# Kernel optimization log

Hardware: AMD Instinct MI355X
Metric: run time of the kernel (lower is better)

The kernel has to match this reference:

```python
import jax, jax.numpy as jnp
import numpy as np

# ---- hyperparameters (from init_kwargs) ----
B, SEQ, D_MODEL = 2, 2048, 1024
D_STATE, D_CONV, EXPAND, HEAD_DIM, CHUNK = 128, 4, 2, 64, 256
D_INNER = EXPAND * D_MODEL            # 2048
NH = D_INNER // HEAD_DIM              # 32 heads
CONV_DIM = D_INNER + 2 * D_STATE      # 2304
D_IN_PROJ = 2 * D_INNER + 2 * D_STATE + NH  # z, xBC, dt -> 4384
D_FF = 4 * D_MODEL
EPS = 1e-12


def setup_inputs() -> dict:
    key = jax.random.key(0)
    ks = jax.random.split(key, 16)
    s = 0.02
    f32 = jnp.float32
    inp = {
        "x": jax.random.normal(ks[0], (B, SEQ, D_MODEL), f32),
        "time_diff": jax.random.uniform(ks[1], (B, SEQ), f32),
        # TiSSD (Mamba2-style) params
        "W_in": jax.random.normal(ks[2], (D_MODEL, D_IN_PROJ), f32) * s,
        "b_in": jnp.zeros((D_IN_PROJ,), f32),
        "conv_w": jax.random.normal(ks[3], (CONV_DIM, D_CONV), f32) * s,
        "conv_b": jnp.zeros((CONV_DIM,), f32),
        "A_log": jnp.log(jnp.arange(1, NH + 1, dtype=f32)),
        "dt_bias": jnp.full((NH,), -2.0, f32),
        "D": jnp.ones((NH,), f32),
        "time_decay": jnp.full((NH,), -3.0, f32),   # time-aware decay rates
        "rms_w": jnp.ones((D_INNER,), f32),
        "W_out": jax.random.normal(ks[4], (D_INNER, D_MODEL), f32) * s,
        "b_out": jnp.zeros((D_MODEL,), f32),
        # wrapper LayerNorm
        "ln_g": jnp.ones((D_MODEL,), f32),
        "ln_b": jnp.zeros((D_MODEL,), f32),
        # FFN
        "fc1_w": jax.random.normal(ks[5], (D_MODEL, D_FF), f32) * s,
        "fc1_b": jnp.zeros((D_FF,), f32),
        "fc2_w": jax.random.normal(ks[6], (D_FF, D_MODEL), f32) * s,
        "fc2_b": jnp.zeros((D_MODEL,), f32),
        "ln2_g": jnp.ones((D_MODEL,), f32),
        "ln2_b": jnp.zeros((D_MODEL,), f32),
    }
    return inp


def _layer_norm(x, g, b, eps=EPS):
    mu = jnp.mean(x, axis=-1, keepdims=True)
    var = jnp.mean(jnp.square(x - mu), axis=-1, keepdims=True)
    return (x - mu) * jax.lax.rsqrt(var + eps) * g + b


def _hardswish(x):
    return x * jnp.clip(x + 3.0, 0.0, 6.0) * (1.0 / 6.0)


def _tissd_forward(x, time_diff, W_in, b_in, conv_w, conv_b, A_log, dt_bias, D,
                   time_decay, rms_w, W_out, b_out):
    b, l, _ = x.shape
    zxbcdt = x @ W_in + b_in                       # [b,l,D_IN_PROJ]
    z = zxbcdt[..., :D_INNER]
    xBC = zxbcdt[..., D_INNER:D_INNER + CONV_DIM]
    dt_raw = zxbcdt[..., -NH:]

    # causal depthwise conv1d (small fixed kernel -> unrolled shifts)
    xp = jnp.pad(xBC, ((0, 0), (D_CONV - 1, 0), (0, 0)))
    xBC_c = conv_b
    for k in range(D_CONV):
        xBC_c = xBC_c + xp[:, k:k + l, :] * conv_w[:, k]
    xBC_c = jax.nn.silu(xBC_c)

    xs = xBC_c[..., :D_INNER]
    Bm = xBC_c[..., D_INNER:D_INNER + D_STATE]     # [b,l,n]
    Cm = xBC_c[..., -D_STATE:]                     # [b,l,n]

    dt = jax.nn.softplus(dt_raw + dt_bias)         # [b,l,h]
    A = -jnp.exp(A_log)                            # [h]
    # time-aware: extra decay proportional to time gap
    dA = dt * A - jax.nn.softplus(time_decay) * time_diff[..., None]  # [b,l,h]

    xh = xs.reshape(b, l, NH, HEAD_DIM)
    xdt = xh * dt[..., None]                       # [b,l,h,p]

    nc = l // CHUNK
    xc = xdt.reshape(b, nc, CHUNK, NH, HEAD_DIM)
    Bc = Bm.reshape(b, nc, CHUNK, D_STATE)
    Cc = Cm.reshape(b, nc, CHUNK, D_STATE)
    dAc = dA.reshape(b, nc, CHUNK, NH).transpose(0, 3, 1, 2)  # [b,h,c,L]

    A_cum = jnp.cumsum(dAc, axis=-1)               # [b,h,c,L]
    seg = A_cum[..., :, None] - A_cum[..., None, :]
    mask = jnp.tril(jnp.ones((CHUNK, CHUNK), bool))
    Lmat = jnp.where(mask, jnp.exp(jnp.where(mask, seg, 0.0)), 0.0)  # [b,h,c,L,L]

    # intra-chunk (diagonal block) output
    Y_diag = jnp.einsum("bcln,bcsn,bhcls,bcshp->bclhp", Cc, Bc, Lmat, xc)

    # per-chunk final states
    decay_states = jnp.exp(A_cum[..., -1:] - A_cum)  # [b,h,c,L]
    states = jnp.einsum("bcln,bhcl,bclhp->bchpn", Bc, decay_states, xc)
    chunk_decay = jnp.exp(A_cum[..., -1])            # [b,h,c]

    # inter-chunk recurrence over nc chunks
    states_t = states.transpose(1, 0, 2, 3, 4)       # [c,b,h,p,n]
    decay_t = chunk_decay.transpose(2, 0, 1)         # [c,b,h]

    def step(carry, inp):
        s_c, d_c = inp
        new = carry * d_c[..., None, None] + s_c
        return new, carry                            # emit state BEFORE chunk

    init = jnp.zeros((b, NH, HEAD_DIM, D_STATE), x.dtype)
    _, prev_states = jax.lax.scan(step, init, (states_t, decay_t))
    prev_states = prev_states.transpose(1, 0, 2, 3, 4)  # [b,c,h,p,n]

    state_decay = jnp.exp(A_cum)                     # [b,h,c,L]
    Y_off = jnp.einsum("bcln,bchpn,bhcl->bclhp", Cc, prev_states, state_decay)

    Y = (Y_diag + Y_off).reshape(b, l, NH, HEAD_DIM) + D[None, None, :, None] * xh
    y = Y.reshape(b, l, D_INNER)

    # gated RMSNorm
    y = y * jax.nn.silu(z)
    y = y * jax.lax.rsqrt(jnp.mean(jnp.square(y), axis=-1, keepdims=True) + EPS) * rms_w
    return y @ W_out + b_out


def reference(x, time_diff, W_in, b_in, conv_w, conv_b, A_log, dt_bias, D,
              time_decay, rms_w, W_out, b_out, ln_g, ln_b,
              fc1_w, fc1_b, fc2_w, fc2_b, ln2_g, ln2_b):
    hidden = _tissd_forward(x, time_diff, W_in, b_in, conv_w, conv_b, A_log,
                            dt_bias, D, time_decay, rms_w, W_out, b_out)
    # num_layers > 1 -> residual; dropout is identity in eval mode
    h = _layer_norm(hidden + x, ln_g, ln_b)
    # FFN with Hardswish and residual LayerNorm
    hid = _hardswish(h @ fc1_w + fc1_b)
    hid = hid @ fc2_w + fc2_b
    out = _layer_norm(hid + h, ln2_g, ln2_b)
    return (out, time_diff)
```

## Files before the change

kernel.cpp:

```cpp
#include <hip/hip_runtime.h>

#define BATCH 2
#define SEQL 2048
#define DM 1024
#define DSTATE 128
#define HD 64
#define CHUNK 256
#define DI 2048
#define NHEADS 32
#define CONVD 2304
#define DPROJ 4384
#define DFF 4096
#define NC 8
#define ROWS (BATCH*SEQL)

typedef unsigned short ushort_t;
typedef short bf16x8 __attribute__((ext_vector_type(8)));
typedef float f32x4 __attribute__((ext_vector_type(4)));

__device__ __forceinline__ float softplus_f(float v){
    return (v > 20.f) ? v : log1pf(expf(v));
}
__device__ __forceinline__ float silu_f(float v){
    return v / (1.f + expf(-v));
}
__device__ __forceinline__ ushort_t f2b(float v){
    union { float f; unsigned int u; } x; x.f = v;
    unsigned int r = x.u + 0x7fffu + ((x.u >> 16) & 1u);
    return (ushort_t)(r >> 16);
}
__device__ __forceinline__ float b2f(ushort_t v){
    union { unsigned int u; float f; } x; x.u = ((unsigned int)v) << 16;
    return x.f;
}

template<int ACT, int OUT_BF16, int TN, int NS, int DTX>
__global__ __launch_bounds__(256) void mfma_gemm_k(
    const ushort_t* __restrict__ A, const ushort_t* __restrict__ Bt,
    const float* __restrict__ bias, float* __restrict__ Cf,
    ushort_t* __restrict__ Cb, float* __restrict__ dtaux,
    int M, int N, int K, int ldc)
{
    constexpr int NT = (TN == 128) ? 4 : 2;
    constexpr int BROWS = TN / 4;
    __shared__ ushort_t As[128*64];
    __shared__ ushort_t Bs[TN*64];
    int tid = threadIdx.x;
    int lane = tid & 63, wave = tid >> 6;
    int m0 = blockIdx.y * 128, n0 = blockIdx.x * TN;
    int Ks = K / NS;
    int kb = (NS > 1) ? blockIdx.z * Ks : 0;
    int wave_m = (TN==128) ? (wave >> 1)*64 : (wave & 1)*64;
    int wave_n = (TN==128) ? (wave & 1)*64 : (wave >> 1)*32;
    int lrow = lane >> 3;
    int lcol = ((lane & 7) ^ lrow) * 8;
    const ushort_t* Abase = A  + (size_t)(m0 + wave*32    + lrow)*K + lcol + kb;
    const ushort_t* Bbase = Bt + (size_t)(n0 + wave*BROWS + lrow)*K + lcol + kb;
    ushort_t* AsW = &As[(wave*32)*64];
    ushort_t* BsW = &Bs[(wave*BROWS)*64];
    f32x4 acc[4][NT];
    #pragma unroll
    for (int i=0;i<4;i++)
        #pragma unroll
        for (int j=0;j<NT;j++) acc[i][j] = (f32x4){0.f,0.f,0.f,0.f};
    int lm = lane & 15;
    int quad = lane >> 4;
    for (int k0 = 0; k0 < Ks; k0 += 64){
        #pragma unroll
        for (int j = 0; j < 4; j++)
            __builtin_amdgcn_global_load_lds(
                (const __attribute__((address_space(1))) void*)(Abase + (size_t)(j*8)*K + k0),
                (__attribute__((address_space(3))) void*)(AsW + j*8*64), 16, 0, 0);
        #pragma unroll
        for (int j = 0; j < BROWS/8; j++)
            __builtin_amdgcn_global_load_lds(
                (const __attribute__((address_space(1))) void*)(Bbase + (size_t)(j*8)*K + k0),
                (__attribute__((address_space(3))) void*)(BsW + j*8*64), 16, 0, 0);
        __syncthreads();
        #pragma unroll
        for (int kk = 0; kk < 64; kk += 32){
            int cb = kk >> 3;
            bf16x8 af[4], bfr[NT];
            #pragma unroll
            for (int mt=0; mt<4; mt++)
                af[mt] = *(const bf16x8*)&As[(wave_m + mt*16 + lm)*64 + (((cb + quad) ^ (lm & 7))*8)];
            #pragma unroll
            for (int nt=0; nt<NT; nt++)
                bfr[nt] = *(const bf16x8*)&Bs[(wave_n + nt*16 + lm)*64 + (((cb + quad) ^ (lm & 7))*8)];
            #pragma unroll
            for (int mt=0; mt<4; mt++)
                #pragma unroll
                for (int nt=0; nt<NT; nt++)
                    acc[mt][nt] = __builtin_amdgcn_mfma_f32_16x16x32_bf16(af[mt], bfr[nt], acc[mt][nt], 0, 0, 0);
        }
        __syncthreads();
    }
    float* Cfo = Cf + (size_t)((NS > 1) ? blockIdx.z : 0) * (size_t)M * ldc;
    int addb = (NS == 1) || (blockIdx.z == 0);
    int crow0 = m0 + wave_m + quad * 4;
    int ccol0 = n0 + wave_n + lm;
    #pragma unroll
    for (int mt=0; mt<4; mt++){
        #pragma unroll
        for (int nt=0; nt<NT; nt++){
            int col = ccol0 + nt*16;
            if (col < N){
                float bv = addb ? bias[col] : 0.f;
                #pragma unroll
                for (int r=0; r<4; r++){
                    int row = crow0 + mt*16 + r;
                    float v = acc[mt][nt][r] + bv;
                    if (ACT == 1){
                        float t = fminf(fmaxf(v + 3.f, 0.f), 6.f);
                        v = v * t * (1.f/6.f);
                    }
                    if (OUT_BF16){
                        Cb[(size_t)row*ldc + col] = f2b(v);
                        if (DTX && col >= N - NHEADS)
                            dtaux[(size_t)row*NHEADS + (col - (N - NHEADS))] = v;
                    } else {
                        Cfo[(size_t)row*ldc + col] = v;
                    }
                }
            }
        }
    }
}

__global__ __launch_bounds__(256) void prep_in_k(const float* __restrict__ x,
                                                 ushort_t* __restrict__ x_bf,
                                                 const float* __restrict__ W_in,
                                                 ushort_t* __restrict__ WinT){
    __shared__ ushort_t tile[32][33];
    int bid = blockIdx.x;
    if (bid < 16384){
        int idx = bid*256 + threadIdx.x;
        x_bf[idx] = f2b(x[idx]);
        return;
    }
    int id2 = bid - 16384;
    int n0 = (id2 % 140)*32, k0 = (id2 / 140)*32;
    int tx = threadIdx.x & 31, ty = threadIdx.x >> 5;
    #pragma unroll
    for (int i = 0; i < 4; i++){
        int k = k0 + ty + i*8;
        int n = n0 + tx;
        float v = (n < DPROJ) ? W_in[(size_t)k*DPROJ + n] : 0.f;
        tile[ty + i*8][tx] = f2b(v);
    }
    __syncthreads();
    #pragma unroll
    for (int i = 0; i < 4; i++)
        WinT[(size_t)(n0 + ty + i*8)*DM + k0 + tx] = tile[tx][ty + i*8];
}

__global__ __launch_bounds__(256) void transpose3_k(const float* __restrict__ Wout,
                                                    const float* __restrict__ fc1w,
                                                    const float* __restrict__ fc2w,
                                                    ushort_t* __restrict__ WoutT,
                                                    ushort_t* __restrict__ fc1T,
                                                    ushort_t* __restrict__ fc2T){
    __shared__ ushort_t tile[32][33];
    int bid = blockIdx.x;
    const float* W; ushort_t* Wt; int K, N, gx, id;
    if (bid < 2048){        W = Wout; Wt = WoutT; K = DI;  N = DM;  gx = 32;  id = bid; }
    else if (bid < 6144){   W = fc1w; Wt = fc1T;  K = DM;  N = DFF; gx = 128; id = bid - 2048; }
    else {                  W = fc2w; Wt = fc2T;  K = DFF; N = DM;  gx = 32;  id = bid - 6144; }
    int n0 = (id % gx)*32, k0 = (id / gx)*32;
    int tx = threadIdx.x & 31, ty = threadIdx.x >> 5;
    #pragma unroll
    for (int i = 0; i < 4; i++){
        int k = k0 + ty + i*8;
        int n = n0 + tx;
        tile[ty + i*8][tx] = f2b(W[(size_t)k*N + n]);
    }
    __syncthreads();
    #pragma unroll
    for (int i = 0; i < 4; i++)
        Wt[(size_t)(n0 + ty + i*8)*K + k0 + tx] = tile[tx][ty + i*8];
}

#define CONVBLKS (ROWS*CONVD/256)
__global__ __launch_bounds__(256) void conv_dt_k(const ushort_t* __restrict__ zx,
                                                 const float* __restrict__ conv_w,
                                                 const float* __restrict__ conv_b,
                                                 ushort_t* __restrict__ convb,
                                                 const float* __restrict__ dtaux,
                                                 const float* __restrict__ time_diff,
                                                 const float* __restrict__ A_log,
                                                 const float* __restrict__ dt_bias,
                                                 const float* __restrict__ time_decay,
                                                 float* __restrict__ dtH,
                                                 float* __restrict__ Acum){
    __shared__ float s[CHUNK];
    int bid = blockIdx.x;
    if (bid < CONVBLKS){
        int idx = bid*256 + threadIdx.x;
        int c = idx % CONVD;
        int row = idx / CONVD;
        int t = row & (SEQL-1);
        float acc = conv_b[c];
        #pragma unroll
        for (int k = 0; k < 4; k++){
            int tt = t + k - 3;
            if (tt >= 0)
                acc += b2f(zx[((size_t)(row + k - 3))*DPROJ + DI + c]) * conv_w[c*4 + k];
        }
        convb[idx] = f2b(silu_f(acc));
        return;
    }
    int id2 = bid - CONVBLKS;
    int c = id2 % NC;
    int h = (id2 / NC) % NHEADS;
    int b = id2 / (NC*NHEADS);
    int l = threadIdx.x;
    int t = c*CHUNK + l;
    float dtr = dtaux[((size_t)(b*SEQL + t))*NHEADS + h];
    float dtv = softplus_f(dtr + dt_bias[h]);
    float A = -expf(A_log[h]);
    float dA = dtv*A - softplus_f(time_decay[h]) * time_diff[b*SEQL + t];
    dtH[((size_t)(b*NHEADS + h))*SEQL + t] = dtv;
    s[l] = dA;
    __syncthreads();
    for (int off = 1; off < CHUNK; off <<= 1){
        float v = (l >= off) ? s[l-off] : 0.f;
        __syncthreads();
        s[l] += v;
        __syncthreads();
    }
    Acum[((size_t)(b*NHEADS + h))*SEQL + t] = s[l];
}

__global__ __launch_bounds__(256) void g_mfma_k(const ushort_t* __restrict__ convb,
                                                ushort_t* __restrict__ G){
    __shared__ ushort_t As[64*136];
    __shared__ ushort_t Bs[64*136];
    int bc = blockIdx.z;
    int l0 = blockIdx.y*64, s0 = blockIdx.x*64;
    int tid = threadIdx.x;
    int lane = tid & 63, wave = tid >> 6;
    int lm = lane & 15, quad = lane >> 4;
    const ushort_t* base = convb + (size_t)bc*CHUNK*CONVD;
    #pragma unroll
    for (int i = 0; i < 4; i++){
        int e = tid + i*256;
        int r = e >> 4, k = (e & 15)*8;
        *(bf16x8*)&As[r*136 + k] = *(const bf16x8*)&base[(size_t)(l0+r)*CONVD + DI + DSTATE + k];
        *(bf16x8*)&Bs[r*136 + k] = *(const bf16x8*)&base[(size_t)(s0+r)*CONVD + DI + k];
    }
    __syncthreads();
    f32x4 acc[4];
    #pragma unroll
    for (int j=0;j<4;j++) acc[j] = (f32x4){0.f,0.f,0.f,0.f};
    #pragma unroll
    for (int kk = 0; kk < 4; kk++){
        bf16x8 af = *(const bf16x8*)&As[(wave*16+lm)*136 + kk*32 + quad*8];
        #pragma unroll
        for (int nt = 0; nt < 4; nt++){
            bf16x8 bfr = *(const bf16x8*)&Bs[(nt*16+lm)*136 + kk*32 + quad*8];
            acc[nt] = __builtin_amdgcn_mfma_f32_16x16x32_bf16(af, bfr, acc[nt], 0, 0, 0);
        }
    }
    ushort_t* g = G + (size_t)bc*CHUNK*CHUNK;
    #pragma unroll
    for (int nt = 0; nt < 4; nt++)
        #pragma unroll
        for (int r = 0; r < 4; r++)
            g[(size_t)(l0 + wave*16 + quad*4 + r)*CHUNK + s0 + nt*16 + lm] = f2b(acc[nt][r]);
}

#define RSX 264
#define RSB 72
__global__ __launch_bounds__(256) void states_mfma_k(const ushort_t* __restrict__ convb,
                                                     const float* __restrict__ dtH,
                                                     const float* __restrict__ Acum,
                                                     float* __restrict__ states){
    __shared__ ushort_t xw[64*RSX];
    __shared__ ushort_t Bt[128*RSB];
    __shared__ float Acs[CHUNK];
    __shared__ float dts[CHUNK];
    int bid = blockIdx.x;
    int h = bid % NHEADS;
    int c = (bid / NHEADS) % NC;
    int b = bid / (NHEADS*NC);
    int tid = threadIdx.x;
    int lane = tid & 63, wave = tid >> 6;
    int lm = lane & 15, quad = lane >> 4;
    Acs[tid] = Acum[((size_t)(b*NHEADS + h))*SEQL + c*CHUNK + tid];
    dts[tid] = dtH[((size_t)(b*NHEADS + h))*SEQL + c*CHUNK + tid];
    __syncthreads();
    float AcL = Acs[CHUNK-1];
    {
        const ushort_t* xg = convb + ((size_t)(b*SEQL + c*CHUNK))*CONVD + h*HD;
        #pragma unroll
        for (int j8 = 0; j8 < 8; j8++){
            int s0 = wave*64 + j8*8;
            bf16x8 pk;
            #pragma unroll
            for (int j = 0; j < 8; j++){
                int l = s0 + j;
                pk[j] = (short)f2b(expf(AcL - Acs[l]) * dts[l] * b2f(xg[(size_t)l*CONVD + lane]));
            }
            *(bf16x8*)&xw[lane*RSX + s0] = pk;
        }
    }
    f32x4 acc[8];
    #pragma unroll
    for (int j=0;j<8;j++) acc[j] = (f32x4){0.f,0.f,0.f,0.f};
    const ushort_t* bbase = convb + ((size_t)(b*SEQL + c*CHUNK))*CONVD + DI;
    for (int l0 = 0; l0 < CHUNK; l0 += 64){
        __syncthreads();
        #pragma unroll
        for (int i = 0; i < 32; i++){
            int e = tid + i*256; int l = e >> 7, n = e & 127;
            Bt[n*RSB + l] = bbase[(size_t)(l0+l)*CONVD + n];
        }
        __syncthreads();
        #pragma unroll
        for (int kk = 0; kk < 2; kk++){
            bf16x8 af = *(const bf16x8*)&xw[(wave*16+lm)*RSX + l0 + kk*32 + quad*8];
            #pragma unroll
            for (int nt = 0; nt < 8; nt++){
                bf16x8 bfr = *(const bf16x8*)&Bt[(nt*16+lm)*RSB + kk*32 + quad*8];
                acc[nt] = __builtin_amdgcn_mfma_f32_16x16x32_bf16(af, bfr, acc[nt], 0, 0, 0);
            }
        }
    }
    float* outp = states + ((size_t)((b*NC + c)*NHEADS + h))*(HD*DSTATE);
    #pragma unroll
    for (int nt = 0; nt < 8; nt++)
        #pragma unroll
        for (int r = 0; r < 4; r++)
            outp[(size_t)(wave*16 + quad*4 + r)*DSTATE + nt*16 + lm] = acc[nt][r];
}

__global__ __launch_bounds__(256) void prev_scan_k(const float* __restrict__ states,
                                                   const float* __restrict__ Acum,
                                                   float* __restrict__ prev){
    int bid = blockIdx.x;
    int part = bid & 15;
    int h = (bid >> 4) & (NHEADS-1);
    int b = bid >> 9;
    int tid = threadIdx.x;
    const float* AcB = Acum + ((size_t)(b*NHEADS + h))*SEQL;
    float dec[NC];
    #pragma unroll
    for (int c = 0; c < NC; c++) dec[c] = expf(AcB[c*CHUNK + CHUNK-1]);
    #pragma unroll
    for (int j = 0; j < 2; j++){
        int e = part*512 + j*256 + tid;
        float carry = 0.f;
        #pragma unroll
        for (int c = 0; c < NC; c++){
            size_t idx = ((size_t)((b*NC + c)*NHEADS + h))*(HD*DSTATE) + e;
            prev[idx] = carry;
            carry = carry*dec[c] + states[idx];
        }
    }
}

#define RLX 264
#define RLP 136
__global__ __launch_bounds__(256) void y_mfma_k(const ushort_t* __restrict__ convb,
                                                const ushort_t* __restrict__ G,
                                                const float* __restrict__ Acum,
                                                const float* __restrict__ dtH,
                                                const float* __restrict__ prev,
                                                const float* __restrict__ Dp,
                                                ushort_t* __restrict__ Ybf){
    __shared__ ushort_t xdtT[64*RLX];
    __shared__ ushort_t prevs[64*RLP];
    __shared__ float Acs[CHUNK];
    __shared__ float dts[CHUNK];
    int bid = blockIdx.x;
    int h = bid % NHEADS;
    int c = (bid / NHEADS) % NC;
    int b = bid / (NHEADS*NC);
    int tid = threadIdx.x;
    int lane = tid & 63, wave = tid >> 6;
    int lm = lane & 15, quad = lane >> 4;

    Acs[tid] = Acum[((size_t)(b*NHEADS + h))*SEQL + c*CHUNK + tid];
    dts[tid] = dtH[((size_t)(b*NHEADS + h))*SEQL + c*CHUNK + tid];
    {
        const float* pv = prev + ((size_t)((b*NC + c)*NHEADS + h))*(HD*DSTATE);
        #pragma unroll
        for (int i = 0; i < 32; i++){
            int e = tid + i*256; int p = e >> 7, n = e & 127;
            prevs[p*RLP + n] = f2b(pv[e]);
        }
    }
    __syncthreads();
    {
        const ushort_t* xg = convb + ((size_t)(b*SEQL + c*CHUNK))*CONVD + h*HD;
        #pragma unroll
        for (int j8 = 0; j8 < 8; j8++){
            int s0 = wave*64 + j8*8;
            bf16x8 pk;
            #pragma unroll
            for (int j = 0; j < 8; j++){
                int l = s0 + j;
                pk[j] = (short)f2b(b2f(xg[(size_t)l*CONVD + lane]) * dts[l]);
            }
            *(bf16x8*)&xdtT[lane*RLX + s0] = pk;
        }
    }
    __syncthreads();

    int   lrow[4];  float Alr[4], eAlr[4];
    #pragma unroll
    for (int mt = 0; mt < 4; mt++){
        lrow[mt] = (mt*4 + wave)*16 + lm;
        Alr[mt]  = Acs[lrow[mt]];
        eAlr[mt] = expf(Alr[mt]);
    }
    const ushort_t* Gbase = G + ((size_t)(b*NC + c))*(CHUNK*CHUNK);

    f32x4 acc[4][4];
    #pragma unroll
    for (int i=0;i<4;i++)
        #pragma unroll
        for (int j=0;j<4;j++) acc[i][j] = (f32x4){0.f,0.f,0.f,0.f};

    for (int ks = 0; ks < 8; ks++){
        bf16x8 bfr[4];
        #pragma unroll
        for (int nt = 0; nt < 4; nt++)
            bfr[nt] = *(const bf16x8*)&xdtT[(nt*16+lm)*RLX + ks*32 + quad*8];
        #pragma unroll
        for (int mt = 0; mt < 4; mt++){
            int rblk = mt*4 + wave;
            int nst = rblk/2 + 1;
            if (ks < nst){
                int sbase = ks*32 + quad*8;
                bf16x8 g8 = *(const bf16x8*)&Gbase[(size_t)lrow[mt]*CHUNK + sbase];
                const float4* A4 = (const float4*)(&Acs[sbase]);
                float4 a0 = A4[0], a1 = A4[1];
                float Al = Alr[mt]; int l = lrow[mt];
                float pv[8];
                pv[0] = (sbase+0 <= l) ? b2f((ushort_t)g8[0])*expf(Al - a0.x) : 0.f;
                pv[1] = (sbase+1 <= l) ? b2f((ushort_t)g8[1])*expf(Al - a0.y) : 0.f;
                pv[2] = (sbase+2 <= l) ? b2f((ushort_t)g8[2])*expf(Al - a0.z) : 0.f;
                pv[3] = (sbase+3 <= l) ? b2f((ushort_t)g8[3])*expf(Al - a0.w) : 0.f;
                pv[4] = (sbase+4 <= l) ? b2f((ushort_t)g8[4])*expf(Al - a1.x) : 0.f;
                pv[5] = (sbase+5 <= l) ? b2f((ushort_t)g8[5])*expf(Al - a1.y) : 0.f;
                pv[6] = (sbase+6 <= l) ? b2f((ushort_t)g8[6])*expf(Al - a1.z) : 0.f;
                pv[7] = (sbase+7 <= l) ? b2f((ushort_t)g8[7])*expf(Al - a1.w) : 0.f;
                bf16x8 af;
                #pragma unroll
                for (int j = 0; j < 8; j++) af[j] = (short)f2b(pv[j]);
                #pragma unroll
                for (int nt = 0; nt < 4; nt++)
                    acc[mt][nt] = __builtin_amdgcn_mfma_f32_16x16x32_bf16(af, bfr[nt], acc[mt][nt], 0, 0, 0);
            }
        }
    }
    for (int kc = 0; kc < 4; kc++){
        bf16x8 bfr[4];
        #pragma unroll
        for (int nt = 0; nt < 4; nt++)
            bfr[nt] = *(const bf16x8*)&prevs[(nt*16+lm)*RLP + kc*32 + quad*8];
        #pragma unroll
        for (int mt = 0; mt < 4; mt++){
            int rowg = b*SEQL + c*CHUNK + lrow[mt];
            bf16x8 c8 = *(const bf16x8*)&convb[(size_t)rowg*CONVD + DI + DSTATE + kc*32 + quad*8];
            float e = eAlr[mt];
            bf16x8 af;
            #pragma unroll
            for (int j = 0; j < 8; j++) af[j] = (short)f2b(e * b2f((ushort_t)c8[j]));
            #pragma unroll
            for (int nt = 0; nt < 4; nt++)
                acc[mt][nt] = __builtin_amdgcn_mfma_f32_16x16x32_bf16(af, bfr[nt], acc[mt][nt], 0, 0, 0);
        }
    }
    float Dv = Dp[h];
    #pragma unroll
    for (int mt = 0; mt < 4; mt++){
        int l0 = (mt*4 + wave)*16 + quad*4;
        #pragma unroll
        for (int nt = 0; nt < 4; nt++){
            int p = nt*16 + lm;
            #pragma unroll
            for (int r = 0; r < 4; r++){
                int rowg = b*SEQL + c*CHUNK + l0 + r;
                float xs = b2f(convb[(size_t)rowg*CONVD + h*HD + p]);
                Ybf[(size_t)rowg*DI + h*HD + p] = f2b(acc[mt][nt][r] + Dv*xs);
            }
        }
    }
}

__global__ __launch_bounds__(256) void gate_rms_k(const ushort_t* __restrict__ Yb,
                                                  const ushort_t* __restrict__ zx,
                                                  const float* __restrict__ rms_w,
                                                  ushort_t* __restrict__ yn){
    __shared__ float red[4];
    __shared__ float scale_s;
    int row = blockIdx.x; int tid = threadIdx.x;
    float v[8]; float ss = 0.f;
    #pragma unroll
    for (int i = 0; i < 8; i++){
        int d = tid + i*256;
        float g = b2f(Yb[(size_t)row*DI + d]) * silu_f(b2f(zx[(size_t)row*DPROJ + d]));
        v[i] = g; ss += g*g;
    }
    #pragma unroll
    for (int off = 32; off > 0; off >>= 1) ss += __shfl_down(ss, off);
    int lane = tid & 63, wid = tid >> 6;
    if (lane == 0) red[wid] = ss;
    __syncthreads();
    if (tid == 0) scale_s = rsqrtf((red[0]+red[1]+red[2]+red[3])*(1.f/DI) + 1e-12f);
    __syncthreads();
    float sc = scale_s;
    #pragma unroll
    for (int i = 0; i < 8; i++){
        int d = tid + i*256;
        yn[(size_t)row*DI + d] = f2b(v[i]*sc*rms_w[d]);
    }
}

__global__ __launch_bounds__(256) void ln_hbf_k(const float* __restrict__ a,
                                                const float* __restrict__ a2,
                                                const float* __restrict__ resid,
                                                const float* __restrict__ g,
                                                const float* __restrict__ bw,
                                                ushort_t* __restrict__ bfout){
    __shared__ float redA[4], redB[4];
    __shared__ float mu_s, rs_s;
    int row = blockIdx.x; int tid = threadIdx.x;
    float u[4]; float s = 0.f, s2 = 0.f;
    #pragma unroll
    for (int i = 0; i < 4; i++){
        int d = tid + i*256;
        float val = a[(size_t)row*DM + d] + a2[(size_t)row*DM + d] + resid[(size_t)row*DM + d];
        u[i] = val; s += val; s2 += val*val;
    }
    #pragma unroll
    for (int off = 32; off > 0; off >>= 1){
        s  += __shfl_down(s,  off);
        s2 += __shfl_down(s2, off);
    }
    int lane = tid & 63, wid = tid >> 6;
    if (lane == 0){ redA[wid] = s; redB[wid] = s2; }
    __syncthreads();
    if (tid == 0){
        float S  = redA[0]+redA[1]+redA[2]+redA[3];
        float S2 = redB[0]+redB[1]+redB[2]+redB[3];
        float mu = S*(1.f/DM);
        float var = S2*(1.f/DM) - mu*mu;
        mu_s = mu; rs_s = rsqrtf(var + 1e-12f);
    }
    __syncthreads();
    float mu = mu_s, rs = rs_s;
    #pragma unroll
    for (int i = 0; i < 4; i++){
        int d = tid + i*256;
        bfout[(size_t)row*DM + d] = f2b((u[i]-mu)*rs*g[d] + bw[d]);
    }
}

__global__ __launch_bounds__(256) void ln_final_k(const float* __restrict__ a,
                                                  const float* __restrict__ a2,
                                                  const ushort_t* __restrict__ residb,
                                                  const float* __restrict__ g,
                                                  const float* __restrict__ bw,
                                                  float* __restrict__ outp,
                                                  const float* __restrict__ td){
    __shared__ float redA[4], redB[4];
    __shared__ float mu_s, rs_s;
    int row = blockIdx.x; int tid = threadIdx.x;
    if (row >= ROWS){
        int idx = (row - ROWS)*256 + tid;
        outp[(size_t)ROWS*DM + idx] = td[idx];
        return;
    }
    float u[4]; float s = 0.f, s2 = 0.f;
    #pragma unroll
    for (int i = 0; i < 4; i++){
        int d = tid + i*256;
        float val = a[(size_t)row*DM + d] + a2[(size_t)row*DM + d] + b2f(residb[(size_t)row*DM + d]);
        u[i] = val; s += val; s2 += val*val;
    }
    #pragma unroll
    for (int off = 32; off > 0; off >>= 1){
        s  += __shfl_down(s,  off);
        s2 += __shfl_down(s2, off);
    }
    int lane = tid & 63, wid = tid >> 6;
    if (lane == 0){ redA[wid] = s; redB[wid] = s2; }
    __syncthreads();
    if (tid == 0){
        float S  = redA[0]+redA[1]+redA[2]+redA[3];
        float S2 = redB[0]+redB[1]+redB[2]+redB[3];
        float mu = S*(1.f/DM);
        float var = S2*(1.f/DM) - mu*mu;
        mu_s = mu; rs_s = rsqrtf(var + 1e-12f);
    }
    __syncthreads();
    float mu = mu_s, rs = rs_s;
    #pragma unroll
    for (int i = 0; i < 4; i++){
        int d = tid + i*256;
        outp[(size_t)row*DM + d] = (u[i]-mu)*rs*g[d] + bw[d];
    }
}

extern "C" void kernel_launch(void* const* d_in, const int* in_sizes, int n_in,
                              void* d_out, int out_size, void* d_ws, size_t ws_size,
                              hipStream_t stream){
    const float* x         = (const float*)d_in[0];
    const float* time_diff = (const float*)d_in[1];
    const float* W_in      = (const float*)d_in[2];
    const float* b_in      = (const float*)d_in[3];
    const float* conv_w    = (const float*)d_in[4];
    const float* conv_b    = (const float*)d_in[5];
    const float* A_log     = (const float*)d_in[6];
    const float* dt_bias   = (const float*)d_in[7];
    const float* Dp        = (const float*)d_in[8];
    const float* time_dec  = (const float*)d_in[9];
    const float* rms_w     = (const float*)d_in[10];
    const float* W_out     = (const float*)d_in[11];
    const float* b_out     = (const float*)d_in[12];
    const float* ln_g      = (const float*)d_in[13];
    const float* ln_b      = (const float*)d_in[14];
    const float* fc1_w     = (const float*)d_in[15];
    const float* fc1_b     = (const float*)d_in[16];
    const float* fc2_w     = (const float*)d_in[17];
    const float* fc2_b     = (const float*)d_in[18];
    const float* ln2_g     = (const float*)d_in[19];
    const float* ln2_b     = (const float*)d_in[20];

    float* ws = (float*)d_ws;
    float* zx    = ws;
    float* convb = zx    + 17956864;
    float* dtH   = convb + 9437184;
    float* Acum  = dtH   + 131072;
    float* r4    = Acum  + 131072;
    float* r5    = r4    + 8388608;
    float* ybreg = r5    + 9437184;
    ushort_t* zx_bf  = (ushort_t*)zx;
    float*    dtaux  = zx + 10600000;
    ushort_t* mid_bf = (ushort_t*)zx;
    ushort_t* h_bf   = (ushort_t*)(zx + 8388608);
    ushort_t* convb_bf = (ushort_t*)convb;
    float* outPa  = convb;
    ushort_t* x_bf  = (ushort_t*)r4;
    ushort_t* WinT  = (ushort_t*)(r4 + 2097152);
    ushort_t* WoutT = (ushort_t*)(r4 + 4194304);
    float* fc2Pa = r4;
    ushort_t* Gb   = (ushort_t*)r5;
    float* stat = r5 + 1048576;
    float* prev = stat + 4194304;
    ushort_t* yn_bf = (ushort_t*)r5;
    ushort_t* fc1T  = (ushort_t*)(r5 + 4194304);
    ushort_t* fc2T  = (ushort_t*)(r5 + 6291456);
    ushort_t* Ybf = (ushort_t*)ybreg;
    float* outp   = (float*)d_out;

    prep_in_k<<<16384 + 4480, 256, 0, stream>>>(x, x_bf, W_in, WinT);
    mfma_gemm_k<0,1,128,1,1><<<dim3(35, ROWS/128), 256, 0, stream>>>(x_bf, WinT, b_in, nullptr, zx_bf, dtaux, ROWS, DPROJ, DM, DPROJ);
    conv_dt_k<<<CONVBLKS + BATCH*NHEADS*NC, 256, 0, stream>>>(zx_bf, conv_w, conv_b, convb_bf,
                                                              dtaux, time_diff, A_log, dt_bias, time_dec, dtH, Acum);
    g_mfma_k<<<dim3(4,4,BATCH*NC), 256, 0, stream>>>(convb_bf, Gb);
    states_mfma_k<<<BATCH*NC*NHEADS, 256, 0, stream>>>(convb_bf, dtH, Acum, stat);
    prev_scan_k<<<BATCH*NHEADS*16, 256, 0, stream>>>(stat, Acum, prev);
    y_mfma_k<<<BATCH*NC*NHEADS, 256, 0, stream>>>(convb_bf, Gb, Acum, dtH, prev, Dp, Ybf);
    gate_rms_k<<<ROWS, 256, 0, stream>>>(Ybf, zx_bf, rms_w, yn_bf);
    transpose3_k<<<10240, 256, 0, stream>>>(W_out, fc1_w, fc2_w, WoutT, fc1T, fc2T);
    mfma_gemm_k<0,0,64,2,0><<<dim3(DM/64, ROWS/128, 2), 256, 0, stream>>>(yn_bf, WoutT, b_out, outPa, nullptr, nullptr, ROWS, DM, DI, DM);
    ln_hbf_k<<<ROWS, 256, 0, stream>>>(outPa, outPa + (size_t)ROWS*DM, x, ln_g, ln_b, h_bf);
    mfma_gemm_k<1,1,128,1,0><<<dim3(DFF/128, ROWS/128), 256, 0, stream>>>(h_bf, fc1T, fc1_b, nullptr, mid_bf, nullptr, ROWS, DFF, DM, DFF);
    mfma_gemm_k<0,0,64,2,0><<<dim3(DM/64, ROWS/128, 2), 256, 0, stream>>>(mid_bf, fc2T, fc2_b, fc2Pa, nullptr, nullptr, ROWS, DM, DFF, DM);
    ln_final_k<<<ROWS + ROWS/256, 256, 0, stream>>>(fc2Pa, fc2Pa + (size_t)ROWS*DM, h_bf, ln2_g, ln2_b, outp, time_diff);
}
```

Measured before the change: 489.7 us.

## Add 256x256 tiled MFMA GEMM with async LDS loads for in-proj and fc1

Adds a 512-thread GEMM kernel with 256x256 output tiles. It double-buffers 64-wide K slices in LDS through global_load_lds direct loads, uses XOR-swizzled LDS addressing, a block-index swizzle for L2 locality, and s_setprio around the MFMA bursts. The in-projection and fc1 GEMMs now use it in place of the 128-tile kernel, and W_in's transpose is padded to 4608 columns so whole 256-wide tiles can be read. This is meant to raise operand reuse and overlap loads with compute, at the cost of heavy register and LDS use per block and grids of only 288 and 256 blocks.

```diff
diff --git a/kernel.cpp b/kernel.cpp
--- a/kernel.cpp
+++ b/kernel.cpp
@@ -10,6 +10,7 @@
 #define NHEADS 32
 #define CONVD 2304
 #define DPROJ 4384
+#define DPROJ_PAD 4608
 #define DFF 4096
 #define NC 8
 #define ROWS (BATCH*SEQL)
@@ -127,6 +128,146 @@
     }
 }
 
+template<int ACT, int DTX>
+__global__ __launch_bounds__(512) void gemm256_k(
+    const ushort_t* __restrict__ A, const ushort_t* __restrict__ Bt,
+    const float* __restrict__ bias, ushort_t* __restrict__ Cb,
+    float* __restrict__ dtaux, int M, int N, int K, int ldc, int nbx)
+{
+    __shared__ ushort_t sm[65536];
+    const int tid  = threadIdx.x;
+    const int lane = tid & 63, wave = tid >> 6;
+    const int lm   = lane & 15, quad = lane >> 4;
+    const int wm   = wave >> 2, wn = wave & 3;
+    const int nwg = gridDim.x;
+    const int cpx = nwg >> 3;
+    const int swz = (blockIdx.x & 7)*cpx + (blockIdx.x >> 3);
+    const int bx = swz % nbx, by = swz / nbx;
+    const int m0 = by << 8, n0 = bx << 8;
+    const int srow = tid >> 2;
+    const int scol = (((tid & 3) ^ ((srow >> 1) & 3)) << 3);
+    const ushort_t* pA = A  + (size_t)(m0 + srow)*K + scol;
+    const ushort_t* pB = Bt + (size_t)(n0 + srow)*K + scol;
+    const size_t rstep = (size_t)128 * K;
+    const int swz8 = ((quad ^ ((lm >> 1) & 3)) << 3);
+    const int aoff = (wm*128 + lm)*32 + swz8;
+    const int boff = 16384 + (wn*64 + lm)*32 + swz8;
+    const int NT = K >> 6;
+
+#define GL(off, src) __builtin_amdgcn_global_load_lds( \
+        (const __attribute__((address_space(1))) void*)(src), \
+        (__attribute__((address_space(3))) void*)(&sm[off]), 16, 0, 0)
+
+    {
+        const int d = wave*512;
+        GL(d,                 pA);        GL(d + 4096,          pA + rstep);
+        GL(d + 16384,         pB);        GL(d + 16384 + 4096,  pB + rstep);
+        GL(d + 8192,          pA + 32);   GL(d + 8192 + 4096,   pA + 32 + rstep);
+        GL(d + 24576,         pB + 32);   GL(d + 24576 + 4096,  pB + 32 + rstep);
+    }
+    asm volatile("s_waitcnt vmcnt(0)" ::: "memory");
+    __builtin_amdgcn_sched_barrier(0);
+    __builtin_amdgcn_s_barrier();
+
+    f32x4 acc[8][4];
+    #pragma unroll
+    for (int i = 0; i < 8; i++)
+        #pragma unroll
+        for (int j = 0; j < 4; j++) acc[i][j] = (f32x4){0.f,0.f,0.f,0.f};
+
+#define MFMA16(MH) \
+    __builtin_amdgcn_s_setprio(1); \
+    _Pragma("unroll") \
+    for (int mt = 0; mt < 4; mt++) \
+        _Pragma("unroll") \
+        for (int nt = 0; nt < 4; nt++) \
+            acc[(MH)*4+mt][nt] = __builtin_amdgcn_mfma_f32_16x16x32_bf16(af[mt], bf[nt], acc[(MH)*4+mt][nt], 0, 0, 0); \
+    __builtin_amdgcn_s_setprio(0);
+
+    for (int t = 0; t < NT; ++t){
+        const int bo = (t & 1) << 15;
+        const int nb = bo ^ 32768;
+        const bool stg = (t < NT-1);
+        const ushort_t* pAn = pA + (size_t)(t+1)*64;
+        const ushort_t* pBn = pB + (size_t)(t+1)*64;
+        bf16x8 af[4], bf[4];
+
+        #pragma unroll
+        for (int nt = 0; nt < 4; nt++) bf[nt] = *(const bf16x8*)&sm[bo + boff + nt*512];
+        #pragma unroll
+        for (int mt = 0; mt < 4; mt++) af[mt] = *(const bf16x8*)&sm[bo + aoff + mt*512];
+        if (stg){ GL(nb + wave*512, pAn); GL(nb + 4096 + wave*512, pAn + rstep); }
+        __builtin_amdgcn_s_barrier();
+        asm volatile("s_waitcnt lgkmcnt(0)");
+        __builtin_amdgcn_sched_barrier(0);
+        MFMA16(0)
+        __builtin_amdgcn_s_barrier();
+
+        #pragma unroll
+        for (int mt = 0; mt < 4; mt++) af[mt] = *(const bf16x8*)&sm[bo + aoff + 2048 + mt*512];
+        if (stg){ GL(nb + 16384 + wave*512, pBn); GL(nb + 16384 + 4096 + wave*512, pBn + rstep); }
+        if (stg) asm volatile("s_waitcnt vmcnt(4)" ::: "memory");
+        else     asm volatile("s_waitcnt vmcnt(0)" ::: "memory");
+        __builtin_amdgcn_sched_barrier(0);
+        __builtin_amdgcn_s_barrier();
+        asm volatile("s_waitcnt lgkmcnt(0)");
+        __builtin_amdgcn_sched_barrier(0);
+        MFMA16(1)
+        __builtin_amdgcn_s_barrier();
+
+        #pragma unroll
+        for (int nt = 0; nt < 4; nt++) bf[nt] = *(const bf16x8*)&sm[bo + 8192 + boff + nt*512];
+        #pragma unroll
+        for (int mt = 0; mt < 4; mt++) af[mt] = *(const bf16x8*)&sm[bo + 8192 + aoff + 2048 + mt*512];
+        if (stg){ GL(nb + 8192 + wave*512, pAn + 32); GL(nb + 8192 + 4096 + wave*512, pAn + 32 + rstep); }
+        __builtin_amdgcn_s_barrier();
+        asm volatile("s_waitcnt lgkmcnt(0)");
+        __builtin_amdgcn_sched_barrier(0);
+        MFMA16(1)
+        __builtin_amdgcn_s_barrier();
+
+        #pragma unroll
+        for (int mt = 0; mt < 4; mt++) af[mt] = *(const bf16x8*)&sm[bo + 8192 + aoff + mt*512];
+        if (stg){
+            GL(nb + 24576 + wave*512, pBn + 32); GL(nb + 24576 + 4096 + wave*512, pBn + 32 + rstep);
+            asm volatile("s_waitcnt vmcnt(4)" ::: "memory");
+            __builtin_amdgcn_sched_barrier(0);
+        }
+        __builtin_amdgcn_s_barrier();
+        asm volatile("s_waitcnt lgkmcnt(0)");
+        __builtin_amdgcn_sched_barrier(0);
+        MFMA16(0)
+        __builtin_amdgcn_s_barrier();
+    }
+#undef MFMA16
+#undef GL
+
+    const int crow = m0 + wm*128 + quad*4;
+    const int ccol = n0 + wn*64 + lm;
+    #pragma unroll
+    for (int m8 = 0; m8 < 8; m8++){
+        #pragma unroll
+        for (int nt = 0; nt < 4; nt++){
+            int col = ccol + nt*16;
+            if (col < N){
+                float bv = bias[col];
+                #pragma unroll
+                for (int r = 0; r < 4; r++){
+                    int row = crow + m8*16 + r;
+                    float v = acc[m8][nt][r] + bv;
+                    if (ACT == 1){
+                        float tt = fminf(fmaxf(v + 3.f, 0.f), 6.f);
+                        v = v * tt * (1.f/6.f);
+                    }
+                    Cb[(size_t)row*ldc + col] = f2b(v);
+                    if (DTX && col >= N - NHEADS)
+                        dtaux[(size_t)row*NHEADS + (col - (N - NHEADS))] = v;
+                }
+            }
+        }
+    }
+}
+
 __global__ __launch_bounds__(256) void prep_in_k(const float* __restrict__ x,
                                                  ushort_t* __restrict__ x_bf,
                                                  const float* __restrict__ W_in,
@@ -139,7 +280,7 @@
         return;
     }
     int id2 = bid - 16384;
-    int n0 = (id2 % 140)*32, k0 = (id2 / 140)*32;
+    int n0 = (id2 % 144)*32, k0 = (id2 / 144)*32;
     int tx = threadIdx.x & 31, ty = threadIdx.x >> 5;
     #pragma unroll
     for (int i = 0; i < 4; i++){
@@ -657,8 +798,8 @@
     ushort_t* Ybf = (ushort_t*)ybreg;
     float* outp   = (float*)d_out;
 
-    prep_in_k<<<16384 + 4480, 256, 0, stream>>>(x, x_bf, W_in, WinT);
-    mfma_gemm_k<0,1,128,1,1><<<dim3(35, ROWS/128), 256, 0, stream>>>(x_bf, WinT, b_in, nullptr, zx_bf, dtaux, ROWS, DPROJ, DM, DPROJ);
+    prep_in_k<<<16384 + 4608, 256, 0, stream>>>(x, x_bf, W_in, WinT);
+    gemm256_k<0,1><<<288, 512, 0, stream>>>(x_bf, WinT, b_in, zx_bf, dtaux, ROWS, DPROJ, DM, DPROJ, 18);
     conv_dt_k<<<CONVBLKS + BATCH*NHEADS*NC, 256, 0, stream>>>(zx_bf, conv_w, conv_b, convb_bf,
                                                               dtaux, time_diff, A_log, dt_bias, time_dec, dtH, Acum);
     g_mfma_k<<<dim3(4,4,BATCH*NC), 256, 0, stream>>>(convb_bf, Gb);
@@ -669,7 +810,7 @@
     transpose3_k<<<10240, 256, 0, stream>>>(W_out, fc1_w, fc2_w, WoutT, fc1T, fc2T);
     mfma_gemm_k<0,0,64,2,0><<<dim3(DM/64, ROWS/128, 2), 256, 0, stream>>>(yn_bf, WoutT, b_out, outPa, nullptr, nullptr, ROWS, DM, DI, DM);
     ln_hbf_k<<<ROWS, 256, 0, stream>>>(outPa, outPa + (size_t)ROWS*DM, x, ln_g, ln_b, h_bf);
-    mfma_gemm_k<1,1,128,1,0><<<dim3(DFF/128, ROWS/128), 256, 0, stream>>>(h_bf, fc1T, fc1_b, nullptr, mid_bf, nullptr, ROWS, DFF, DM, DFF);
+    gemm256_k<1,0><<<256, 512, 0, stream>>>(h_bf, fc1T, fc1_b, mid_bf, nullptr, ROWS, DFF, DM, DFF, 16);
     mfma_gemm_k<0,0,64,2,0><<<dim3(DM/64, ROWS/128, 2), 256, 0, stream>>>(mid_bf, fc2T, fc2_b, fc2Pa, nullptr, nullptr, ROWS, DM, DFF, DM);
     ln_final_k<<<ROWS + ROWS/256, 256, 0, stream>>>(fc2Pa, fc2Pa + (size_t)ROWS*DM, h_bf, ln2_g, ln2_b, outp, time_diff);
 }
```

After: 480.4 us. Within noise of the previous version (-1.9%).
